# Kernel tuning notes

Hardware: AMD Instinct MI355X
Metric: run time of the kernel (lower is better)

Reference implementation:

```python
import jax, jax.numpy as jnp
import numpy as np

NUM_HEADS = 12


def setup_inputs() -> dict:
    key = jax.random.key(0)
    k1, k2, k3, k4 = jax.random.split(key, 4)
    B, N, C = 8, 1024, 768
    x = jax.random.normal(k1, (B, N, C), dtype=jnp.float32)
    w_qkv = jax.random.normal(k2, (3 * C, C), dtype=jnp.float32) * 0.02
    w_proj = jax.random.normal(k3, (C, C), dtype=jnp.float32) * 0.02
    b_proj = jax.random.normal(k4, (C,), dtype=jnp.float32) * 0.02
    return {"x": x, "w_qkv": w_qkv, "w_proj": w_proj, "b_proj": b_proj}


def reference(x, w_qkv, w_proj, b_proj):
    B, N, C = x.shape
    H = NUM_HEADS
    D = C // H
    scale = D ** -0.5
    # qkv projection (HMQLinear with quant=False is a plain linear, bias=False)
    qkv = jnp.einsum('bnc,oc->bno', x, w_qkv)          # [B,N,3C]
    qkv = qkv.reshape(B, N, 3, H, D).transpose(2, 0, 3, 1, 4)  # [3,B,H,N,D]
    q, k, v = qkv[0], qkv[1], qkv[2]
    # HMQMulQK (passthrough matmul), scale applied after QK^T as in source
    attn = jnp.einsum('bhqd,bhkd->bhqk', q, k) * scale  # [B,H,N,N]
    attn = jax.nn.softmax(attn, axis=-1)                # HMQSoftmax
    out = jnp.einsum('bhqk,bhkd->bhqd', attn, v)        # HMQMulSV
    out = out.transpose(0, 2, 1, 3).reshape(B, N, C)
    # output projection (HMQLinear, default bias=True)
    return jnp.einsum('bnc,oc->bno', out, w_proj) + b_proj
```

## Files before the change

### kernel.cpp

```cpp
#include <hip/hip_runtime.h>
#include <hip/hip_bf16.h>
#include <stdint.h>

typedef __attribute__((ext_vector_type(8))) short short8;
typedef __attribute__((ext_vector_type(4))) float f32x4;
typedef __attribute__((ext_vector_type(16))) float f32x16;
typedef __attribute__((ext_vector_type(4))) unsigned short us4;

__device__ inline unsigned short f2bf(float f) {
    unsigned int u = __float_as_uint(f);
    u += 0x7FFFu + ((u >> 16) & 1u);
    return (unsigned short)(u >> 16);
}

__device__ inline unsigned int cvtpk(float lo, float hi) {
    unsigned int r;
    asm("v_cvt_pk_bf16_f32 %0, %1, %2" : "=v"(r) : "v"(lo), "v"(hi));
    return r;
}

__device__ inline void pl32swap(unsigned int& a, unsigned int& b) {
    asm volatile("v_permlane32_swap_b32 %0, %1" : "+v"(a), "+v"(b));
}

__device__ inline float fexp2(float x) {
#if __has_builtin(__builtin_amdgcn_exp2f)
    return __builtin_amdgcn_exp2f(x);
#else
    return exp2f(x);
#endif
}

__global__ void cvt_all(const float* __restrict__ x, const float* __restrict__ wq,
                        const float* __restrict__ wp,
                        unsigned short* __restrict__ xb,
                        unsigned short* __restrict__ wqb,
                        unsigned short* __restrict__ wpb) {
    const int X4 = 1572864, Q4 = 442368;
    int i = blockIdx.x * blockDim.x + threadIdx.x;
    const float* src; unsigned short* dst; int j;
    if (i < X4) { src = x; dst = xb; j = i; }
    else if (i < X4 + Q4) { src = wq; dst = wqb; j = i - X4; }
    else { src = wp; dst = wpb; j = i - X4 - Q4; }
    float4 v = ((const float4*)src)[j];
    us4 o;
    o.x = f2bf(v.x); o.y = f2bf(v.y); o.z = f2bf(v.z); o.w = f2bf(v.w);
    ((us4*)dst)[j] = o;
}

#define BM 128
#define BN 128
#define BKK 32

template<int MODE>
__global__ __launch_bounds__(256)
void gemm_bt(const unsigned short* __restrict__ A,
             const unsigned short* __restrict__ Bm,
             unsigned short* __restrict__ Qo, unsigned short* __restrict__ Ko,
             unsigned short* __restrict__ Vto,
             float* __restrict__ Co, const float* __restrict__ bias,
             int M, int N, int K)
{
    __shared__ __align__(16) unsigned short As[2][BM * BKK];
    __shared__ __align__(16) unsigned short Bs[2][BN * BKK];
    const int tid = threadIdx.x;
    const int wave = tid >> 6, lane = tid & 63;
    const int tr = blockIdx.x * BM;
    const int tc = blockIdx.y * BN;
    const int wm = wave >> 1, wn = wave & 1;

    f32x4 acc[4][4] = {};

    const int srow = lane >> 2;
    const int scol = (lane & 3) * 8;

    auto stage = [&](int it, int buf) {
#pragma unroll
        for (int i = 0; i < 2; ++i) {
            int rb = (wave * 2 + i) * 16;
            __builtin_amdgcn_global_load_lds(
                (const __attribute__((address_space(1))) void*)(A + (size_t)(tr + rb + srow) * K + it * BKK + scol),
                (__attribute__((address_space(3))) void*)(&As[buf][rb * BKK]),
                16, 0, 0);
            __builtin_amdgcn_global_load_lds(
                (const __attribute__((address_space(1))) void*)(Bm + (size_t)(tc + rb + srow) * K + it * BKK + scol),
                (__attribute__((address_space(3))) void*)(&Bs[buf][rb * BKK]),
                16, 0, 0);
        }
    };

    const int nIt = K / BKK;
    stage(0, 0);
    __syncthreads();

    for (int it = 0; it < nIt; ++it) {
        const int cur = it & 1;
        if (it + 1 < nIt) stage(it + 1, cur ^ 1);

        short8 af[4], bf[4];
#pragma unroll
        for (int mt = 0; mt < 4; ++mt)
            af[mt] = *(const short8*)&As[cur][(wm * 64 + mt * 16 + (lane & 15)) * BKK + (lane >> 4) * 8];
#pragma unroll
        for (int nt = 0; nt < 4; ++nt)
            bf[nt] = *(const short8*)&Bs[cur][(wn * 64 + nt * 16 + (lane & 15)) * BKK + (lane >> 4) * 8];
#pragma unroll
        for (int mt = 0; mt < 4; ++mt)
#pragma unroll
            for (int nt = 0; nt < 4; ++nt)
                acc[mt][nt] = __builtin_amdgcn_mfma_f32_16x16x32_bf16(af[mt], bf[nt], acc[mt][nt], 0, 0, 0);
        __syncthreads();
    }

    const float QSCALE = 0.18033688011112042f;
#pragma unroll
    for (int mt = 0; mt < 4; ++mt) {
#pragma unroll
        for (int nt = 0; nt < 4; ++nt) {
            int col = tc + wn * 64 + nt * 16 + (lane & 15);
            int row0 = tr + wm * 64 + mt * 16 + (lane >> 4) * 4;
            if constexpr (MODE == 0) {
                int s = (col >= 1536) ? 2 : (col >= 768 ? 1 : 0);
                int rem = col - s * 768;
                int h = rem >> 6, d = rem & 63;
                int b = row0 >> 10, n0 = row0 & 1023;
                int bh = b * 12 + h;
                if (s == 2) {
                    us4 pv;
#pragma unroll
                    for (int r = 0; r < 4; ++r) pv[r] = f2bf(acc[mt][nt][r]);
                    int qd = (n0 >> 2) & 3;
                    int nst = n0 + ((qd == 1) ? 4 : (qd == 2) ? -4 : 0);
                    *(us4*)&Vto[((size_t)bh * 64 + d) * 1024 + nst] = pv;
                } else {
                    unsigned short* dst = (s == 0) ? Qo : Ko;
                    float sc = (s == 0) ? QSCALE : 1.0f;
#pragma unroll
                    for (int r = 0; r < 4; ++r)
                        dst[((size_t)bh * 1024 + n0 + r) * 64 + d] = f2bf(acc[mt][nt][r] * sc);
                }
            } else {
#pragma unroll
                for (int r = 0; r < 4; ++r)
                    Co[(size_t)(row0 + r) * N + col] = acc[mt][nt][r] + bias[col];
            }
        }
    }
}

__global__ __launch_bounds__(256, 3)
void attn_kernel(const unsigned short* __restrict__ Q,
                 const unsigned short* __restrict__ Kg,
                 const unsigned short* __restrict__ Vt,
                 unsigned short* __restrict__ Og)
{
    __shared__ __align__(16) unsigned short KV[2][2][64 * 64];

    const int tid = threadIdx.x;
    const int wave = tid >> 6, lane = tid & 63;
    const int l31 = lane & 31, hi = lane >> 5;
    const int bh = blockIdx.y;
    const int b = bh / 12, h = bh % 12;
    const size_t baseK = (size_t)bh * 1024 * 64;
    const size_t baseV = (size_t)bh * 64 * 1024;
    const int q0 = blockIdx.x * 128 + wave * 32;

    short8 qf[4];
#pragma unroll
    for (int ds = 0; ds < 4; ++ds)
        qf[ds] = *(const short8*)&Q[baseK + (size_t)(q0 + l31) * 64 + ds * 16 + hi * 8];

    f32x16 ot0 = {}, ot1 = {};
    float l = 0.f;

    auto stage = [&](int kt, int buf) {
        const unsigned short* gK = Kg + baseK + (size_t)kt * 64 * 64;
        const unsigned short* gV = Vt + baseV + kt * 64;
#pragma unroll
        for (int i = 0; i < 2; ++i) {
            int c = wave * 128 + i * 64 + lane;
            int r = c >> 3, cc = c & 7;
            int sw = (cc ^ (r & 7)) * 8;
            __builtin_amdgcn_global_load_lds(
                (const __attribute__((address_space(1))) void*)(gK + r * 64 + sw),
                (__attribute__((address_space(3))) void*)(&KV[buf][0][(wave * 128 + i * 64) * 8]),
                16, 0, 0);
            __builtin_amdgcn_global_load_lds(
                (const __attribute__((address_space(1))) void*)(gV + (size_t)r * 1024 + sw),
                (__attribute__((address_space(3))) void*)(&KV[buf][1][(wave * 128 + i * 64) * 8]),
                16, 0, 0);
        }
    };

    auto rfrag = [&](const unsigned short* s, int row, int cc) -> short8 {
        return *(const short8*)&s[(row * 8 + (cc ^ (row & 7))) * 8];
    };

    auto pack8 = [&](const f32x16& S, int r0) -> short8 {
        union { unsigned int u[4]; short8 s; } fr;
#pragma unroll
        for (int w = 0; w < 4; ++w)
            fr.u[w] = cvtpk(S[r0 + 2 * w], S[r0 + 2 * w + 1]);
        return fr.s;
    };

    stage(0, 0);
    __syncthreads();

    for (int kt = 0; kt < 16; ++kt) {
        const int cur = kt & 1;
        if (kt < 15) stage(kt + 1, cur ^ 1);

        f32x16 st0 = {}, st1 = {};
        __builtin_amdgcn_s_setprio(1);
#pragma unroll
        for (int ds = 0; ds < 4; ++ds) {
            short8 k0 = rfrag(KV[cur][0], l31, ds * 2 + hi);
            short8 k1 = rfrag(KV[cur][0], 32 + l31, ds * 2 + hi);
            st0 = __builtin_amdgcn_mfma_f32_32x32x16_bf16(k0, qf[ds], st0, 0, 0, 0);
            st1 = __builtin_amdgcn_mfma_f32_32x32x16_bf16(k1, qf[ds], st1, 0, 0, 0);
        }
        __builtin_amdgcn_s_setprio(0);

        short8 v00 = rfrag(KV[cur][1], l31, 0 + hi);
        short8 v10 = rfrag(KV[cur][1], 32 + l31, 0 + hi);
        short8 v01 = rfrag(KV[cur][1], l31, 2 + hi);
        short8 v11 = rfrag(KV[cur][1], 32 + l31, 2 + hi);

#pragma unroll
        for (int i = 0; i < 16; ++i) st0[i] = fexp2(st0[i]);
        short8 paf0 = pack8(st0, 0);
        short8 paf1 = pack8(st0, 8);

        __builtin_amdgcn_s_setprio(1);
        ot0 = __builtin_amdgcn_mfma_f32_32x32x16_bf16(v00, paf0, ot0, 0, 0, 0);
        ot1 = __builtin_amdgcn_mfma_f32_32x32x16_bf16(v10, paf0, ot1, 0, 0, 0);
        ot0 = __builtin_amdgcn_mfma_f32_32x32x16_bf16(v01, paf1, ot0, 0, 0, 0);
        ot1 = __builtin_amdgcn_mfma_f32_32x32x16_bf16(v11, paf1, ot1, 0, 0, 0);
        __builtin_amdgcn_s_setprio(0);

        short8 v02 = rfrag(KV[cur][1], l31, 4 + hi);
        short8 v12 = rfrag(KV[cur][1], 32 + l31, 4 + hi);
        short8 v03 = rfrag(KV[cur][1], l31, 6 + hi);
        short8 v13 = rfrag(KV[cur][1], 32 + l31, 6 + hi);
#pragma unroll
        for (int i = 0; i < 16; ++i) st1[i] = fexp2(st1[i]);
        short8 paf2 = pack8(st1, 0);
        short8 paf3 = pack8(st1, 8);

        __builtin_amdgcn_s_setprio(1);
        ot0 = __builtin_amdgcn_mfma_f32_32x32x16_bf16(v02, paf2, ot0, 0, 0, 0);
        ot1 = __builtin_amdgcn_mfma_f32_32x32x16_bf16(v12, paf2, ot1, 0, 0, 0);
        ot0 = __builtin_amdgcn_mfma_f32_32x32x16_bf16(v03, paf3, ot0, 0, 0, 0);
        ot1 = __builtin_amdgcn_mfma_f32_32x32x16_bf16(v13, paf3, ot1, 0, 0, 0);
        __builtin_amdgcn_s_setprio(0);

        float su[8];
#pragma unroll
        for (int i = 0; i < 8; ++i)
            su[i] = (st0[2 * i] + st0[2 * i + 1]) + (st1[2 * i] + st1[2 * i + 1]);
#pragma unroll
        for (int s = 4; s > 0; s >>= 1)
#pragma unroll
            for (int i = 0; i < 4; ++i)
                if (i < s) su[i] += su[i + s];
        l += su[0];

        __syncthreads();
    }

    {
        unsigned int pu = __float_as_uint(l), pv = pu;
        pl32swap(pu, pv);
        l += __uint_as_float(hi ? pv : pu);
    }

    float inv = 1.f / l;
#pragma unroll
    for (int i = 0; i < 16; ++i) { ot0[i] *= inv; ot1[i] *= inv; }

    unsigned int* ow = (unsigned int*)(&KV[0][0][0]) + wave * 1152;
#pragma unroll
    for (int dt = 0; dt < 2; ++dt)
#pragma unroll
        for (int rp = 0; rp < 8; ++rp) {
            unsigned int w = (dt == 0) ? cvtpk(ot0[2 * rp], ot0[2 * rp + 1])
                                       : cvtpk(ot1[2 * rp], ot1[2 * rp + 1]);
            int wd = dt * 16 + 4 * (rp >> 1) + 2 * hi + (rp & 1);
            ow[l31 * 36 + wd] = w;
        }
#pragma unroll
    for (int i = 0; i < 4; ++i) {
        int c = i * 64 + lane;
        int qr = c >> 3, ch = c & 7;
        short8 vv = *(const short8*)((const unsigned short*)&ow[qr * 36 + ch * 4]);
        *(short8*)&Og[(size_t)(b * 1024 + q0 + qr) * 768 + h * 64 + ch * 8] = vv;
    }
}

extern "C" void kernel_launch(void* const* d_in, const int* in_sizes, int n_in,
                              void* d_out, int out_size, void* d_ws, size_t ws_size,
                              hipStream_t stream) {
    const float* x      = (const float*)d_in[0];
    const float* w_qkv  = (const float*)d_in[1];
    const float* w_proj = (const float*)d_in[2];
    const float* b_proj = (const float*)d_in[3];
    float* out = (float*)d_out;

    const int Bb = 8, Nn = 1024, C = 768;
    const int M = Bb * Nn;
    const size_t XB = (size_t)M * C;
    const size_t WQ = (size_t)3 * C * C;
    const size_t WP = (size_t)C * C;
    const size_t QE = (size_t)96 * 1024 * 64;

    unsigned short* xb  = (unsigned short*)d_ws;
    unsigned short* wqb = xb + XB;
    unsigned short* wpb = wqb + WQ;
    unsigned short* Qb  = wpb + WP;
    unsigned short* Kb  = Qb + QE;
    unsigned short* Vtb = Kb + QE;
    unsigned short* AO  = Vtb + QE;

    cvt_all<<<8448, 256, 0, stream>>>(x, w_qkv, w_proj, xb, wqb, wpb);

    gemm_bt<0><<<dim3(M / BM, (3 * C) / BN), 256, 0, stream>>>(
        xb, wqb, Qb, Kb, Vtb, nullptr, nullptr, M, 3 * C, C);

    attn_kernel<<<dim3(Nn / 128, Bb * 12), 256, 0, stream>>>(Qb, Kb, Vtb, AO);

    gemm_bt<1><<<dim3(M / BM, C / BN), 256, 0, stream>>>(
        AO, wpb, nullptr, nullptr, nullptr, out, b_proj, M, C, C);
}
```

Measured before the change: 116.3 us.

## Replace QKV GEMM with 256x256-tile, 8-wave pipelined kernel using swizzled LDS

Replaces the generic 128x128 QKV projection GEMM with a dedicated 256x256-tile kernel using 512 threads, BK=64 and XOR-swizzled LDS. It splits each K step into four quadrant MFMA phases, interleaving prefetch of the next tile's quarters with explicit vmcnt waits, barriers and setprio around the MFMA bursts. The goal is higher data reuse per LDS load, fewer bank conflicts, and overlap of global-to-LDS copies with compute. The cost is much larger LDS use (128KB per block), fewer resident blocks, and fragile hand-tuned wait counts. The output projection keeps the old kernel under a new name.

```diff
diff --git a/kernel.cpp b/kernel.cpp
--- a/kernel.cpp
+++ b/kernel.cpp
@@ -6,6 +6,9 @@
 typedef __attribute__((ext_vector_type(4))) float f32x4;
 typedef __attribute__((ext_vector_type(16))) float f32x16;
 typedef __attribute__((ext_vector_type(4))) unsigned short us4;
+
+#define AS1 __attribute__((address_space(1)))
+#define AS3 __attribute__((address_space(3)))
 
 __device__ inline unsigned short f2bf(float f) {
     unsigned int u = __float_as_uint(f);
@@ -30,6 +33,11 @@
     return exp2f(x);
 #endif
 }
+
+#define VMW(N) asm volatile("s_waitcnt vmcnt(" #N ")" ::: "memory")
+#define LGK0() do { asm volatile("s_waitcnt lgkmcnt(0)" ::: "memory"); \
+                    __builtin_amdgcn_sched_barrier(0); } while (0)
+#define BARR() __builtin_amdgcn_s_barrier()
 
 __global__ void cvt_all(const float* __restrict__ x, const float* __restrict__ wq,
                         const float* __restrict__ wp,
@@ -48,18 +56,157 @@
     ((us4*)dst)[j] = o;
 }
 
+#define MFMA_Q(MH, NH)                                                        \
+    __builtin_amdgcn_s_setprio(1);                                            \
+    _Pragma("unroll")                                                         \
+    for (int mt = 0; mt < 4; ++mt) {                                          \
+        _Pragma("unroll")                                                     \
+        for (int nt = 0; nt < 2; ++nt) {                                      \
+            acc[MH][NH][mt][nt] = __builtin_amdgcn_mfma_f32_16x16x32_bf16(    \
+                af[mt][0], bf[NH][nt][0], acc[MH][NH][mt][nt], 0, 0, 0);      \
+            acc[MH][NH][mt][nt] = __builtin_amdgcn_mfma_f32_16x16x32_bf16(    \
+                af[mt][1], bf[NH][nt][1], acc[MH][NH][mt][nt], 0, 0, 0);      \
+        }                                                                     \
+    }                                                                         \
+    __builtin_amdgcn_s_setprio(0);
+
+__global__ __launch_bounds__(512, 2)
+void qkv_gemm(const unsigned short* __restrict__ Ag,
+              const unsigned short* __restrict__ Bg,
+              unsigned short* __restrict__ Qo, unsigned short* __restrict__ Ko,
+              unsigned short* __restrict__ Vto)
+{
+    __shared__ __align__(16) unsigned short ldsA[2][2][128 * 64];
+    __shared__ __align__(16) unsigned short ldsB[2][2][128 * 64];
+    const int tid = threadIdx.x;
+    const int wave = tid >> 6, lane = tid & 63;
+    const int wm = wave >> 2, wn = wave & 3;
+    const int tr = blockIdx.x * 256, tc = blockIdx.y * 256;
+    const int K = 768;
+
+    f32x4 acc[2][2][4][2] = {};
+    short8 af[4][2];
+    short8 bf[2][2][2];
+
+    auto stA = [&](int t, int buf, int mh) {
+#pragma unroll
+        for (int i = 0; i < 2; ++i) {
+            int cid = i * 512 + tid;
+            int r = cid >> 3, cd = cid & 7;
+            int sc = cd ^ (r & 7);
+            __builtin_amdgcn_global_load_lds(
+                (const AS1 void*)(Ag + (size_t)(tr + mh * 128 + r) * K + t * 64 + sc * 8),
+                (AS3 void*)(&ldsA[buf][mh][(i * 512 + wave * 64) * 8]),
+                16, 0, 0);
+        }
+    };
+    auto stB = [&](int t, int buf, int nh) {
+#pragma unroll
+        for (int i = 0; i < 2; ++i) {
+            int cid = i * 512 + tid;
+            int r = cid >> 3, cd = cid & 7;
+            int sc = cd ^ (r & 7);
+            __builtin_amdgcn_global_load_lds(
+                (const AS1 void*)(Bg + (size_t)(tc + nh * 128 + r) * K + t * 64 + sc * 8),
+                (AS3 void*)(&ldsB[buf][nh][(i * 512 + wave * 64) * 8]),
+                16, 0, 0);
+        }
+    };
+    auto rdA = [&](int buf, int mh, int mt, int kk) -> short8 {
+        int rr = wm * 64 + mt * 16 + (lane & 15);
+        int pc = (kk * 4 + (lane >> 4)) ^ (lane & 7);
+        return *(const short8*)&ldsA[buf][mh][rr * 64 + pc * 8];
+    };
+    auto rdB = [&](int buf, int nh, int nt, int kk) -> short8 {
+        int rr = wn * 32 + nt * 16 + (lane & 15);
+        int pc = (kk * 4 + (lane >> 4)) ^ (lane & 7);
+        return *(const short8*)&ldsB[buf][nh][rr * 64 + pc * 8];
+    };
+
+    stA(0, 0, 0); stB(0, 0, 0); stB(0, 0, 1); stA(0, 0, 1);
+    VMW(4);
+    BARR();
+
+    for (int t = 0; t < 12; ++t) {
+        const int b = t & 1, nb = b ^ 1;
+        const bool pf = (t < 11);
+#pragma unroll
+        for (int mt = 0; mt < 4; ++mt) {
+            af[mt][0] = rdA(b, 0, mt, 0);
+            af[mt][1] = rdA(b, 0, mt, 1);
+        }
+#pragma unroll
+        for (int nt = 0; nt < 2; ++nt) {
+            bf[0][nt][0] = rdB(b, 0, nt, 0);
+            bf[0][nt][1] = rdB(b, 0, nt, 1);
+        }
+        if (pf) { stA(t + 1, nb, 0); VMW(4); } else { VMW(2); }
+        BARR(); LGK0();
+        MFMA_Q(0, 0);
+#pragma unroll
+        for (int nt = 0; nt < 2; ++nt) {
+            bf[1][nt][0] = rdB(b, 1, nt, 0);
+            bf[1][nt][1] = rdB(b, 1, nt, 1);
+        }
+        if (pf) { stB(t + 1, nb, 0); VMW(4); } else { VMW(0); }
+        BARR(); LGK0();
+        MFMA_Q(0, 1);
+#pragma unroll
+        for (int mt = 0; mt < 4; ++mt) {
+            af[mt][0] = rdA(b, 1, mt, 0);
+            af[mt][1] = rdA(b, 1, mt, 1);
+        }
+        if (pf) stB(t + 1, nb, 1);
+        BARR(); LGK0();
+        MFMA_Q(1, 0);
+        if (pf) { stA(t + 1, nb, 1); VMW(4); }
+        BARR();
+        MFMA_Q(1, 1);
+    }
+
+    const float QSCALE = 0.18033688011112042f;
+    const int s = blockIdx.y / 3;
+#pragma unroll
+    for (int mh = 0; mh < 2; ++mh)
+#pragma unroll
+    for (int nh = 0; nh < 2; ++nh)
+#pragma unroll
+    for (int mt = 0; mt < 4; ++mt)
+#pragma unroll
+    for (int nt = 0; nt < 2; ++nt) {
+        int col = tc + wn * 32 + nh * 128 + nt * 16 + (lane & 15);
+        int row0 = tr + wm * 64 + mh * 128 + mt * 16 + (lane >> 4) * 4;
+        int rem = col - s * 768;
+        int h = rem >> 6, d = rem & 63;
+        int bb = row0 >> 10, n0 = row0 & 1023;
+        int bh = bb * 12 + h;
+        f32x4 v = acc[mh][nh][mt][nt];
+        if (s == 2) {
+            us4 pv;
+#pragma unroll
+            for (int r = 0; r < 4; ++r) pv[r] = f2bf(v[r]);
+            int qd = (n0 >> 2) & 3;
+            int nst = n0 + ((qd == 1) ? 4 : (qd == 2) ? -4 : 0);
+            *(us4*)&Vto[((size_t)bh * 64 + d) * 1024 + nst] = pv;
+        } else {
+            unsigned short* dst = s ? Ko : Qo;
+            float sc2 = s ? 1.0f : QSCALE;
+#pragma unroll
+            for (int r = 0; r < 4; ++r)
+                dst[((size_t)bh * 1024 + n0 + r) * 64 + d] = f2bf(v[r] * sc2);
+        }
+    }
+}
+
 #define BM 128
 #define BN 128
 #define BKK 32
 
-template<int MODE>
 __global__ __launch_bounds__(256)
-void gemm_bt(const unsigned short* __restrict__ A,
-             const unsigned short* __restrict__ Bm,
-             unsigned short* __restrict__ Qo, unsigned short* __restrict__ Ko,
-             unsigned short* __restrict__ Vto,
-             float* __restrict__ Co, const float* __restrict__ bias,
-             int M, int N, int K)
+void proj_gemm(const unsigned short* __restrict__ A,
+               const unsigned short* __restrict__ Bm,
+               float* __restrict__ Co, const float* __restrict__ bias,
+               int M, int N, int K)
 {
     __shared__ __align__(16) unsigned short As[2][BM * BKK];
     __shared__ __align__(16) unsigned short Bs[2][BN * BKK];
@@ -79,13 +226,11 @@
         for (int i = 0; i < 2; ++i) {
             int rb = (wave * 2 + i) * 16;
             __builtin_amdgcn_global_load_lds(
-                (const __attribute__((address_space(1))) void*)(A + (size_t)(tr + rb + srow) * K + it * BKK + scol),
-                (__attribute__((address_space(3))) void*)(&As[buf][rb * BKK]),
-                16, 0, 0);
-            __builtin_amdgcn_global_load_lds(
-                (const __attribute__((address_space(1))) void*)(Bm + (size_t)(tc + rb + srow) * K + it * BKK + scol),
-                (__attribute__((address_space(3))) void*)(&Bs[buf][rb * BKK]),
-                16, 0, 0);
+                (const AS1 void*)(A + (size_t)(tr + rb + srow) * K + it * BKK + scol),
+                (AS3 void*)(&As[buf][rb * BKK]), 16, 0, 0);
+            __builtin_amdgcn_global_load_lds(
+                (const AS1 void*)(Bm + (size_t)(tc + rb + srow) * K + it * BKK + scol),
+                (AS3 void*)(&Bs[buf][rb * BKK]), 16, 0, 0);
         }
     };
 
@@ -97,55 +242,31 @@
         const int cur = it & 1;
         if (it + 1 < nIt) stage(it + 1, cur ^ 1);
 
-        short8 af[4], bf[4];
+        short8 af[4], bfr[4];
 #pragma unroll
         for (int mt = 0; mt < 4; ++mt)
             af[mt] = *(const short8*)&As[cur][(wm * 64 + mt * 16 + (lane & 15)) * BKK + (lane >> 4) * 8];
 #pragma unroll
         for (int nt = 0; nt < 4; ++nt)
-            bf[nt] = *(const short8*)&Bs[cur][(wn * 64 + nt * 16 + (lane & 15)) * BKK + (lane >> 4) * 8];
+            bfr[nt] = *(const short8*)&Bs[cur][(wn * 64 + nt * 16 + (lane & 15)) * BKK + (lane >> 4) * 8];
 #pragma unroll
         for (int mt = 0; mt < 4; ++mt)
 #pragma unroll
             for (int nt = 0; nt < 4; ++nt)
-                acc[mt][nt] = __builtin_amdgcn_mfma_f32_16x16x32_bf16(af[mt], bf[nt], acc[mt][nt], 0, 0, 0);
+                acc[mt][nt] = __builtin_amdgcn_mfma_f32_16x16x32_bf16(af[mt], bfr[nt], acc[mt][nt], 0, 0, 0);
         __syncthreads();
     }
 
-    const float QSCALE = 0.18033688011112042f;
-#pragma unroll
-    for (int mt = 0; mt < 4; ++mt) {
+#pragma unroll
+    for (int mt = 0; mt < 4; ++mt)
 #pragma unroll
         for (int nt = 0; nt < 4; ++nt) {
             int col = tc + wn * 64 + nt * 16 + (lane & 15);
             int row0 = tr + wm * 64 + mt * 16 + (lane >> 4) * 4;
-            if constexpr (MODE == 0) {
-                int s = (col >= 1536) ? 2 : (col >= 768 ? 1 : 0);
-                int rem = col - s * 768;
-                int h = rem >> 6, d = rem & 63;
-                int b = row0 >> 10, n0 = row0 & 1023;
-                int bh = b * 12 + h;
-                if (s == 2) {
-                    us4 pv;
-#pragma unroll
-                    for (int r = 0; r < 4; ++r) pv[r] = f2bf(acc[mt][nt][r]);
-                    int qd = (n0 >> 2) & 3;
-                    int nst = n0 + ((qd == 1) ? 4 : (qd == 2) ? -4 : 0);
-                    *(us4*)&Vto[((size_t)bh * 64 + d) * 1024 + nst] = pv;
-                } else {
-                    unsigned short* dst = (s == 0) ? Qo : Ko;
-                    float sc = (s == 0) ? QSCALE : 1.0f;
-#pragma unroll
-                    for (int r = 0; r < 4; ++r)
-                        dst[((size_t)bh * 1024 + n0 + r) * 64 + d] = f2bf(acc[mt][nt][r] * sc);
-                }
-            } else {
-#pragma unroll
-                for (int r = 0; r < 4; ++r)
-                    Co[(size_t)(row0 + r) * N + col] = acc[mt][nt][r] + bias[col];
-            }
-        }
-    }
+#pragma unroll
+            for (int r = 0; r < 4; ++r)
+                Co[(size_t)(row0 + r) * N + col] = acc[mt][nt][r] + bias[col];
+        }
 }
 
 __global__ __launch_bounds__(256, 3)
@@ -182,13 +303,11 @@
             int r = c >> 3, cc = c & 7;
             int sw = (cc ^ (r & 7)) * 8;
             __builtin_amdgcn_global_load_lds(
-                (const __attribute__((address_space(1))) void*)(gK + r * 64 + sw),
-                (__attribute__((address_space(3))) void*)(&KV[buf][0][(wave * 128 + i * 64) * 8]),
-                16, 0, 0);
-            __builtin_amdgcn_global_load_lds(
-                (const __attribute__((address_space(1))) void*)(gV + (size_t)r * 1024 + sw),
-                (__attribute__((address_space(3))) void*)(&KV[buf][1][(wave * 128 + i * 64) * 8]),
-                16, 0, 0);
+                (const AS1 void*)(gK + r * 64 + sw),
+                (AS3 void*)(&KV[buf][0][(wave * 128 + i * 64) * 8]), 16, 0, 0);
+            __builtin_amdgcn_global_load_lds(
+                (const AS1 void*)(gV + (size_t)r * 1024 + sw),
+                (AS3 void*)(&KV[buf][1][(wave * 128 + i * 64) * 8]), 16, 0, 0);
         }
     };
 
@@ -324,11 +443,11 @@
 
     cvt_all<<<8448, 256, 0, stream>>>(x, w_qkv, w_proj, xb, wqb, wpb);
 
-    gemm_bt<0><<<dim3(M / BM, (3 * C) / BN), 256, 0, stream>>>(
-        xb, wqb, Qb, Kb, Vtb, nullptr, nullptr, M, 3 * C, C);
+    qkv_gemm<<<dim3(M / 256, (3 * C) / 256), 512, 0, stream>>>(
+        xb, wqb, Qb, Kb, Vtb);
 
     attn_kernel<<<dim3(Nn / 128, Bb * 12), 256, 0, stream>>>(Qb, Kb, Vtb, AO);
 
-    gemm_bt<1><<<dim3(M / BM, C / BN), 256, 0, stream>>>(
-        AO, wpb, nullptr, nullptr, nullptr, out, b_proj, M, C, C);
-}
+    proj_gemm<<<dim3(M / BM, C / BN), 256, 0, stream>>>(
+        AO, wpb, out, b_proj, M, C, C);
+}
```

Measured after the change: 120.8 us. 1.04x slower.

## Overlap next-tile loads with compute via partial vmcnt waits and swizzle GEMM LDS

Applied to the files above, without the earlier changes.

Replaces __syncthreads (which drains all outstanding loads) with raw s_barrier plus s_waitcnt vmcnt(4), so the prefetch of the next tile stays in flight while the current tile is consumed, in both the GEMM and attention loops. The GEMM staging layout also gets an XOR swizzle on LDS chunk columns, meant to cut bank conflicts on fragment reads. The approach relies on the compiler not reordering or adding other vector-memory ops, since the vmcnt value is hand-counted.

```diff
diff --git a/kernel.cpp b/kernel.cpp
--- a/kernel.cpp
+++ b/kernel.cpp
@@ -6,6 +6,9 @@
 typedef __attribute__((ext_vector_type(4))) float f32x4;
 typedef __attribute__((ext_vector_type(16))) float f32x16;
 typedef __attribute__((ext_vector_type(4))) unsigned short us4;
+
+#define AS1 __attribute__((address_space(1)))
+#define AS3 __attribute__((address_space(3)))
 
 __device__ inline unsigned short f2bf(float f) {
     unsigned int u = __float_as_uint(f);
@@ -30,6 +33,9 @@
     return exp2f(x);
 #endif
 }
+
+#define VMW(N) asm volatile("s_waitcnt vmcnt(" #N ")" ::: "memory")
+#define BARR() __builtin_amdgcn_s_barrier()
 
 __global__ void cvt_all(const float* __restrict__ x, const float* __restrict__ wq,
                         const float* __restrict__ wp,
@@ -50,7 +56,6 @@
 
 #define BM 128
 #define BN 128
-#define BKK 32
 
 template<int MODE>
 __global__ __launch_bounds__(256)
@@ -61,8 +66,8 @@
              float* __restrict__ Co, const float* __restrict__ bias,
              int M, int N, int K)
 {
-    __shared__ __align__(16) unsigned short As[2][BM * BKK];
-    __shared__ __align__(16) unsigned short Bs[2][BN * BKK];
+    __shared__ __align__(16) unsigned short As[2][BM * 32];
+    __shared__ __align__(16) unsigned short Bs[2][BM * 32];
     const int tid = threadIdx.x;
     const int wave = tid >> 6, lane = tid & 63;
     const int tr = blockIdx.x * BM;
@@ -71,45 +76,48 @@
 
     f32x4 acc[4][4] = {};
 
-    const int srow = lane >> 2;
-    const int scol = (lane & 3) * 8;
-
     auto stage = [&](int it, int buf) {
 #pragma unroll
         for (int i = 0; i < 2; ++i) {
-            int rb = (wave * 2 + i) * 16;
+            int cid = i * 256 + tid;
+            int r = cid >> 2, cd = cid & 3;
+            int sc = cd ^ (r & 3);
             __builtin_amdgcn_global_load_lds(
-                (const __attribute__((address_space(1))) void*)(A + (size_t)(tr + rb + srow) * K + it * BKK + scol),
-                (__attribute__((address_space(3))) void*)(&As[buf][rb * BKK]),
-                16, 0, 0);
+                (const AS1 void*)(A + (size_t)(tr + r) * K + it * 32 + sc * 8),
+                (AS3 void*)(&As[buf][(i * 256 + wave * 64) * 8]), 16, 0, 0);
             __builtin_amdgcn_global_load_lds(
-                (const __attribute__((address_space(1))) void*)(Bm + (size_t)(tc + rb + srow) * K + it * BKK + scol),
-                (__attribute__((address_space(3))) void*)(&Bs[buf][rb * BKK]),
-                16, 0, 0);
+                (const AS1 void*)(Bm + (size_t)(tc + r) * K + it * 32 + sc * 8),
+                (AS3 void*)(&Bs[buf][(i * 256 + wave * 64) * 8]), 16, 0, 0);
         }
     };
 
-    const int nIt = K / BKK;
+    const int nIt = K / 32;
     stage(0, 0);
-    __syncthreads();
 
     for (int it = 0; it < nIt; ++it) {
         const int cur = it & 1;
-        if (it + 1 < nIt) stage(it + 1, cur ^ 1);
-
-        short8 af[4], bf[4];
+        if (it + 1 < nIt) { stage(it + 1, cur ^ 1); VMW(4); }
+        else              { VMW(0); }
+        BARR();
+
+        short8 af[4], bfr[4];
+#pragma unroll
+        for (int mt = 0; mt < 4; ++mt) {
+            int rr = wm * 64 + mt * 16 + (lane & 15);
+            af[mt] = *(const short8*)&As[cur][rr * 32 + (((lane >> 4) ^ (rr & 3)) * 8)];
+        }
+#pragma unroll
+        for (int nt = 0; nt < 4; ++nt) {
+            int rr = wn * 64 + nt * 16 + (lane & 15);
+            bfr[nt] = *(const short8*)&Bs[cur][rr * 32 + (((lane >> 4) ^ (rr & 3)) * 8)];
+        }
 #pragma unroll
         for (int mt = 0; mt < 4; ++mt)
-            af[mt] = *(const short8*)&As[cur][(wm * 64 + mt * 16 + (lane & 15)) * BKK + (lane >> 4) * 8];
-#pragma unroll
-        for (int nt = 0; nt < 4; ++nt)
-            bf[nt] = *(const short8*)&Bs[cur][(wn * 64 + nt * 16 + (lane & 15)) * BKK + (lane >> 4) * 8];
-#pragma unroll
-        for (int mt = 0; mt < 4; ++mt)
 #pragma unroll
             for (int nt = 0; nt < 4; ++nt)
-                acc[mt][nt] = __builtin_amdgcn_mfma_f32_16x16x32_bf16(af[mt], bf[nt], acc[mt][nt], 0, 0, 0);
-        __syncthreads();
+                acc[mt][nt] = __builtin_amdgcn_mfma_f32_16x16x32_bf16(af[mt], bfr[nt], acc[mt][nt], 0, 0, 0);
+
+        BARR();
     }
 
     const float QSCALE = 0.18033688011112042f;
@@ -182,13 +190,11 @@
             int r = c >> 3, cc = c & 7;
             int sw = (cc ^ (r & 7)) * 8;
             __builtin_amdgcn_global_load_lds(
-                (const __attribute__((address_space(1))) void*)(gK + r * 64 + sw),
-                (__attribute__((address_space(3))) void*)(&KV[buf][0][(wave * 128 + i * 64) * 8]),
-                16, 0, 0);
+                (const AS1 void*)(gK + r * 64 + sw),
+                (AS3 void*)(&KV[buf][0][(wave * 128 + i * 64) * 8]), 16, 0, 0);
             __builtin_amdgcn_global_load_lds(
-                (const __attribute__((address_space(1))) void*)(gV + (size_t)r * 1024 + sw),
-                (__attribute__((address_space(3))) void*)(&KV[buf][1][(wave * 128 + i * 64) * 8]),
-                16, 0, 0);
+                (const AS1 void*)(gV + (size_t)r * 1024 + sw),
+                (AS3 void*)(&KV[buf][1][(wave * 128 + i * 64) * 8]), 16, 0, 0);
         }
     };
 
@@ -205,11 +211,12 @@
     };
 
     stage(0, 0);
-    __syncthreads();
 
     for (int kt = 0; kt < 16; ++kt) {
         const int cur = kt & 1;
-        if (kt < 15) stage(kt + 1, cur ^ 1);
+        if (kt < 15) { stage(kt + 1, cur ^ 1); VMW(4); }
+        else         { VMW(0); }
+        BARR();
 
         f32x16 st0 = {}, st1 = {};
         __builtin_amdgcn_s_setprio(1);
@@ -266,7 +273,7 @@
                 if (i < s) su[i] += su[i + s];
         l += su[0];
 
-        __syncthreads();
+        BARR();
     }
 
     {
```

New measurement: 116.1 us. Within noise of the previous version (-0.2%).
